# Performance work log

Hardware: AMD Instinct MI355X
Metric: run time of the kernel (lower is better)

Reference implementation:

```python
import jax, jax.numpy as jnp
import numpy as np

V, B, T, D, H, C = 50000, 64, 256, 256, 256, 32  # H = hidden_dim//2 per direction


def setup_inputs() -> dict:
    key = jax.random.key(0)
    ks = jax.random.split(key, 16)
    u = lambda k, s, a=0.1: jax.random.uniform(k, s, jnp.float32, -a, a)
    sc = 1.0 / float(np.sqrt(H))             # pytorch LSTM init range
    xav = float(np.sqrt(6.0 / (2 * H + C)))  # xavier_uniform for hidden2tag
    inp = {}
    inp['sentences'] = jax.random.randint(ks[0], (B, T), 1, V).astype(jnp.int32)
    inp['lengths'] = jax.random.randint(ks[1], (B,), 1, T + 1).astype(jnp.int32)
    inp['emb'] = u(ks[2], (V, D))
    inp['w_ih_f'] = u(ks[3], (4 * H, D), sc)
    inp['w_hh_f'] = u(ks[4], (4 * H, H), sc)
    inp['b_ih_f'] = u(ks[5], (4 * H,), sc)
    inp['b_hh_f'] = u(ks[6], (4 * H,), sc)
    inp['w_ih_b'] = u(ks[7], (4 * H, D), sc)
    inp['w_hh_b'] = u(ks[8], (4 * H, H), sc)
    inp['b_ih_b'] = u(ks[9], (4 * H,), sc)
    inp['b_hh_b'] = u(ks[10], (4 * H,), sc)
    inp['w_out'] = u(ks[11], (C, 2 * H), xav)
    inp['b_out'] = jnp.zeros((C,), jnp.float32)
    inp['start_trans'] = u(ks[12], (C,))
    inp['end_trans'] = u(ks[13], (C,))
    inp['trans'] = u(ks[14], (C, C))
    return inp


def _lstm(x, w_ih, w_hh, b_ih, b_hh):
    # x: [B,T,In] -> outputs [B,T,H]; PyTorch gate order i,f,g,o
    Bn, Hn = x.shape[0], w_hh.shape[1]

    def step(carry, x_t):
        h, c = carry
        g = x_t @ w_ih.T + h @ w_hh.T + (b_ih + b_hh)
        i, f, gg, o = jnp.split(g, 4, axis=-1)
        c = jax.nn.sigmoid(f) * c + jax.nn.sigmoid(i) * jnp.tanh(gg)
        h = jax.nn.sigmoid(o) * jnp.tanh(c)
        return (h, c), h

    init = (jnp.zeros((Bn, Hn), x.dtype), jnp.zeros((Bn, Hn), x.dtype))
    _, hs = jax.lax.scan(step, init, jnp.swapaxes(x, 0, 1))
    return jnp.swapaxes(hs, 0, 1)


def _emissions(sentences, lengths, emb, w_ih_f, w_hh_f, b_ih_f, b_hh_f,
               w_ih_b, w_hh_b, b_ih_b, b_hh_b, w_out, b_out):
    x = emb[sentences]                       # [B,T,D]
    Tn = x.shape[1]
    out_f = _lstm(x, w_ih_f, w_hh_f, b_ih_f, b_hh_f)
    # packed BiLSTM reverses each sequence within its own length
    t_idx = jnp.arange(Tn)
    rev = jnp.where(t_idx[None, :] < lengths[:, None],
                    lengths[:, None] - 1 - t_idx[None, :], t_idx[None, :])
    x_rev = jnp.take_along_axis(x, rev[:, :, None], axis=1)
    out_b = _lstm(x_rev, w_ih_b, w_hh_b, b_ih_b, b_hh_b)
    out_b = jnp.take_along_axis(out_b, rev[:, :, None], axis=1)  # rev is involution on valid region
    h = jnp.concatenate([out_f, out_b], axis=-1)  # [B,T,2H]
    return h @ w_out.T + b_out                    # [B,T,C]


def _viterbi(emissions, mask, lengths, start_trans, end_trans, trans):
    Bn, Tn, Cn = emissions.shape
    em = jnp.swapaxes(emissions, 0, 1)  # [T,B,C]
    mk = jnp.swapaxes(mask, 0, 1)       # [T,B]
    score0 = start_trans + em[0]

    def step(score, xs):
        emit_t, m_t = xs
        cand = score[:, :, None] + trans            # [B,C_prev,C_cur]
        best_prev = jnp.argmax(cand, axis=1)        # [B,C]
        new = jnp.where(m_t[:, None], jnp.max(cand, axis=1) + emit_t, score)
        return new, best_prev

    final, hist = jax.lax.scan(step, score0, (em[1:], mk[1:]))
    final = final + end_trans
    best_last = jnp.argmax(final, axis=1)           # [B]
    best_score = jnp.max(final, axis=1)             # [B]
    bidx = jnp.arange(Bn)

    def back(tag, xs):
        h_t, t = xs
        new = jnp.where(t < lengths - 1, h_t[bidx, tag], tag)
        return new, new

    _, tags = jax.lax.scan(back, best_last, (hist, jnp.arange(Tn - 1)), reverse=True)
    paths = jnp.concatenate([tags, best_last[None]], axis=0).T  # [B,T]; entries past length hold best_last
    return paths, best_score


def reference(sentences, lengths, emb, w_ih_f, w_hh_f, b_ih_f, b_hh_f,
              w_ih_b, w_hh_b, b_ih_b, b_hh_b, w_out, b_out,
              start_trans, end_trans, trans):
    mask = jnp.arange(sentences.shape[1])[None, :] < lengths[:, None]
    emissions = _emissions(sentences, lengths, emb, w_ih_f, w_hh_f, b_ih_f, b_hh_f,
                           w_ih_b, w_hh_b, b_ih_b, b_hh_b, w_out, b_out)
    return _viterbi(emissions, mask, lengths, start_trans, end_trans, trans)
```

## Files before the change

kernel.cpp:

```cpp
#include <hip/hip_runtime.h>
#include <math.h>


typedef unsigned long long ull;

__device__ __forceinline__ void bar_lds()
{
    asm volatile("s_waitcnt lgkmcnt(0)\n\ts_barrier" ::: "memory");
}

__global__ __launch_bounds__(256) void k1_xgemm(
    const int* __restrict__ sent, const int* __restrict__ lens,
    const float* __restrict__ emb,
    const float* __restrict__ wih_f, const float* __restrict__ wih_b,
    const float* __restrict__ bih_f, const float* __restrict__ bhh_f,
    const float* __restrict__ bih_b, const float* __restrict__ bhh_b,
    float* __restrict__ xg)
{
    const int bid = blockIdx.x;
    const int dir = bid >> 10;
    const int rem = bid & 1023;
    const int mt = rem >> 3, nt = rem & 7;
    const int r0 = mt * 128, j0 = nt * 128;
    const int b = r0 >> 8, t0 = r0 & 255;
    const float* __restrict__ wih = dir ? wih_b : wih_f;
    const float* __restrict__ bih = dir ? bih_b : bih_f;
    const float* __restrict__ bhh = dir ? bhh_b : bhh_f;

    __shared__ __align__(16) float At[32][132];
    __shared__ __align__(16) float Bt[32][132];
    __shared__ int tok_s[128];

    const int tid = threadIdx.x;
    if (tid < 128) {
        int t = t0 + tid;
        int tt = t;
        if (dir) { int L = lens[b]; if (t < L) tt = L - 1 - t; }
        tok_s[tid] = sent[b * 256 + tt];
    }
    __syncthreads();

    float acc[8][8];
    #pragma unroll
    for (int i = 0; i < 8; ++i)
        #pragma unroll
        for (int j = 0; j < 8; ++j) acc[i][j] = 0.f;

    const int lrow = tid >> 3;
    const int l8 = tid & 7;
    const int tx = tid & 15, ty = tid >> 4;

    for (int kc = 0; kc < 256; kc += 32) {
        #pragma unroll
        for (int it = 0; it < 4; ++it) {
            int row = lrow + it * 32;
            float4 va = *(const float4*)(emb + (size_t)tok_s[row] * 256 + kc + l8 * 4);
            At[l8*4+0][row] = va.x; At[l8*4+1][row] = va.y;
            At[l8*4+2][row] = va.z; At[l8*4+3][row] = va.w;
            float4 vb = *(const float4*)(wih + (size_t)(j0 + row) * 256 + kc + l8 * 4);
            Bt[l8*4+0][row] = vb.x; Bt[l8*4+1][row] = vb.y;
            Bt[l8*4+2][row] = vb.z; Bt[l8*4+3][row] = vb.w;
        }
        __syncthreads();
        #pragma unroll
        for (int k = 0; k < 32; ++k) {
            float4 a0 = *(const float4*)&At[k][ty*8];
            float4 a1 = *(const float4*)&At[k][ty*8+4];
            float4 b0 = *(const float4*)&Bt[k][tx*8];
            float4 b1 = *(const float4*)&Bt[k][tx*8+4];
            float av[8] = {a0.x,a0.y,a0.z,a0.w,a1.x,a1.y,a1.z,a1.w};
            float bv[8] = {b0.x,b0.y,b0.z,b0.w,b1.x,b1.y,b1.z,b1.w};
            #pragma unroll
            for (int i = 0; i < 8; ++i)
                #pragma unroll
                for (int j = 0; j < 8; ++j)
                    acc[i][j] += av[i] * bv[j];
        }
        __syncthreads();
    }

    float bias[8];
    {
        float4 p0 = *(const float4*)(bih + j0 + tx*8);
        float4 p1 = *(const float4*)(bih + j0 + tx*8 + 4);
        float4 q0 = *(const float4*)(bhh + j0 + tx*8);
        float4 q1 = *(const float4*)(bhh + j0 + tx*8 + 4);
        bias[0]=p0.x+q0.x; bias[1]=p0.y+q0.y; bias[2]=p0.z+q0.z; bias[3]=p0.w+q0.w;
        bias[4]=p1.x+q1.x; bias[5]=p1.y+q1.y; bias[6]=p1.z+q1.z; bias[7]=p1.w+q1.w;
    }
    #pragma unroll
    for (int i = 0; i < 8; ++i) {
        int r = r0 + ty*8 + i;
        int t = r & 255;
        float* orow = xg + ((size_t)(dir*64 + b) * 256 + t) * 1024 + j0 + tx*8;
        float4 o0, o1;
        o0.x = acc[i][0]+bias[0]; o0.y = acc[i][1]+bias[1];
        o0.z = acc[i][2]+bias[2]; o0.w = acc[i][3]+bias[3];
        o1.x = acc[i][4]+bias[4]; o1.y = acc[i][5]+bias[5];
        o1.z = acc[i][6]+bias[6]; o1.w = acc[i][7]+bias[7];
        *(float4*)orow = o0;
        *(float4*)(orow + 4) = o1;
    }
}

__global__ __launch_bounds__(512)
__attribute__((amdgpu_waves_per_eu(2, 2)))
void k2_lstm(
    const float* __restrict__ whh_f, const float* __restrict__ whh_b,
    const float* __restrict__ xg, float* __restrict__ hcat,
    ull* __restrict__ hx)
{
    const int m = blockIdx.x >> 6;
    const int g = blockIdx.x & 63;
    const int dir = g >> 5;
    const int b0 = (g & 31) * 2;
    const float* __restrict__ w = dir ? whh_b : whh_f;

    const int tid = threadIdx.x;
    const int kg = tid >> 6;
    const int q  = tid & 63;
    const int gate = q >> 4;
    const int u0 = (q & 15) * 4;
    const int kbase = kg * 32;
    const int j0 = gate * 256 + m * 64 + u0;

    float4 wv[4][8];
    #pragma unroll
    for (int j = 0; j < 4; ++j) {
        const float* wp = w + (size_t)(j0 + j) * 256 + kbase;
        #pragma unroll
        for (int i = 0; i < 8; ++i)
            wv[j][i] = *(const float4*)(wp + i * 4);
    }
    #pragma unroll
    for (int j = 0; j < 4; ++j)
        #pragma unroll
        for (int i = 0; i < 8; ++i)
            asm volatile("" : "+v"(wv[j][i].x), "+v"(wv[j][i].y),
                              "+v"(wv[j][i].z), "+v"(wv[j][i].w));

    __shared__ __align__(16) float hs[2][256];
    __shared__ __align__(16) float red[8][2][256];

    const int s_c = tid >> 6, ul = tid & 63;
    const float* xgp = xg + (size_t)(dir * 64 + b0 + s_c) * 262144 + m * 64 + ul;
    ull* hx_w = hx + ((size_t)g * 2 + s_c) * 256 + m * 64 + ul;
    float* hc_w = hcat + (size_t)(b0 + s_c) * 131072 + dir * 256 + m * 64 + ul;

    const int tid2 = tid - 256;
    const int s_r = tid2 >> 7, pr = tid2 & 127;
    const ull* hx_r = hx + ((size_t)g * 2 + s_r) * 256 + 2 * pr;

    ((float*)hs)[tid & 511] = 0.f;
    float c_reg = 0.f;
    bar_lds();

    for (int t = 0; t < 256; ++t) {
        const int par = t & 1;

        float xp0 = 0.f, xp1 = 0.f, xp2 = 0.f, xp3 = 0.f;
        if (tid < 128) {
            const float* xq = xgp + (size_t)t * 1024;
            xp0 = xq[0]; xp1 = xq[256]; xp2 = xq[512]; xp3 = xq[768];
        }

        float a0s0 = 0.f, a1s0 = 0.f, a2s0 = 0.f, a3s0 = 0.f;
        float a0s1 = 0.f, a1s1 = 0.f, a2s1 = 0.f, a3s1 = 0.f;
        #pragma unroll
        for (int i = 0; i < 8; ++i) {
            float4 ha = *(const float4*)&hs[0][kbase + i * 4];
            float4 hb = *(const float4*)&hs[1][kbase + i * 4];
            float4 w0 = wv[0][i], w1 = wv[1][i], w2 = wv[2][i], w3 = wv[3][i];
            a0s0 += w0.x*ha.x + w0.y*ha.y + w0.z*ha.z + w0.w*ha.w;
            a1s0 += w1.x*ha.x + w1.y*ha.y + w1.z*ha.z + w1.w*ha.w;
            a2s0 += w2.x*ha.x + w2.y*ha.y + w2.z*ha.z + w2.w*ha.w;
            a3s0 += w3.x*ha.x + w3.y*ha.y + w3.z*ha.z + w3.w*ha.w;
            a0s1 += w0.x*hb.x + w0.y*hb.y + w0.z*hb.z + w0.w*hb.w;
            a1s1 += w1.x*hb.x + w1.y*hb.y + w1.z*hb.z + w1.w*hb.w;
            a2s1 += w2.x*hb.x + w2.y*hb.y + w2.z*hb.z + w2.w*hb.w;
            a3s1 += w3.x*hb.x + w3.y*hb.y + w3.z*hb.z + w3.w*hb.w;
        }
        float4 r0v; r0v.x = a0s0; r0v.y = a1s0; r0v.z = a2s0; r0v.w = a3s0;
        float4 r1v; r1v.x = a0s1; r1v.y = a1s1; r1v.z = a2s1; r1v.w = a3s1;
        *(float4*)&red[kg][0][q * 4] = r0v;
        *(float4*)&red[kg][1][q * 4] = r1v;
        bar_lds();

        if (tid < 128) {
            float gi = xp0, gf = xp1, gg = xp2, go = xp3;
            #pragma unroll
            for (int kk = 0; kk < 8; ++kk) {
                gi += red[kk][s_c][ul];
                gf += red[kk][s_c][64 + ul];
                gg += red[kk][s_c][128 + ul];
                go += red[kk][s_c][192 + ul];
            }
            float si = 1.f / (1.f + expf(-gi));
            float sf = 1.f / (1.f + expf(-gf));
            float so = 1.f / (1.f + expf(-go));
            c_reg = sf * c_reg + si * tanhf(gg);
            float hn = so * tanhf(c_reg);
            ull pk = ((ull)(unsigned)(t + 1) << 32) | (ull)__float_as_uint(hn);
            __hip_atomic_store(hx_w + (size_t)par * 32768, pk,
                               __ATOMIC_RELAXED, __HIP_MEMORY_SCOPE_AGENT);
            hc_w[(size_t)t * 512] = hn;
        } else if (tid >= 256) {
            const unsigned tg = (unsigned)(t + 1);
            const ull* p = hx_r + (size_t)par * 32768;
            ull v0, v1;
            do {
                v0 = __hip_atomic_load(p,     __ATOMIC_RELAXED, __HIP_MEMORY_SCOPE_AGENT);
                v1 = __hip_atomic_load(p + 1, __ATOMIC_RELAXED, __HIP_MEMORY_SCOPE_AGENT);
            } while ((unsigned)(v0 >> 32) != tg || (unsigned)(v1 >> 32) != tg);
            hs[s_r][2 * pr]     = __uint_as_float((unsigned)v0);
            hs[s_r][2 * pr + 1] = __uint_as_float((unsigned)v1);
        }
        bar_lds();
    }
}

__global__ __launch_bounds__(256) void k3_emis(
    const float* __restrict__ hcat, const float* __restrict__ wout,
    const float* __restrict__ bout, const int* __restrict__ lens,
    float* __restrict__ em)
{
    const int b = blockIdx.x >> 3;
    const int tt0 = (blockIdx.x & 7) * 32;
    __shared__ float wsw[512 * 32];
    const int tid = threadIdx.x;
    for (int i = tid; i < 16384; i += 256) {
        int c_ = i >> 9, k_ = i & 511;
        wsw[k_ * 32 + ((k_ + c_) & 31)] = wout[i];
    }
    __syncthreads();
    const int c = tid & 31, tq = tid >> 5;
    const int L = lens[b];
    float acc[4];
    const float* hfp[4];
    const float* hbp[4];
    int tv[4];
    #pragma unroll
    for (int i = 0; i < 4; ++i) {
        int t = tt0 + i * 8 + tq;
        tv[i] = t;
        int tr = (t < L) ? (L - 1 - t) : t;
        hfp[i] = hcat + ((size_t)b * 256 + t) * 512;
        hbp[i] = hcat + ((size_t)b * 256 + tr) * 512 + 256;
        acc[i] = bout[c];
    }
    for (int k = 0; k < 256; k += 4) {
        float w0 = wsw[(k+0)*32 + ((k+0+c)&31)];
        float w1 = wsw[(k+1)*32 + ((k+1+c)&31)];
        float w2_ = wsw[(k+2)*32 + ((k+2+c)&31)];
        float w3 = wsw[(k+3)*32 + ((k+3+c)&31)];
        #pragma unroll
        for (int i = 0; i < 4; ++i) {
            float4 h = *(const float4*)(hfp[i] + k);
            acc[i] += h.x*w0 + h.y*w1 + h.z*w2_ + h.w*w3;
        }
        float v0 = wsw[(256+k+0)*32 + ((256+k+0+c)&31)];
        float v1 = wsw[(256+k+1)*32 + ((256+k+1+c)&31)];
        float v2 = wsw[(256+k+2)*32 + ((256+k+2+c)&31)];
        float v3 = wsw[(256+k+3)*32 + ((256+k+3+c)&31)];
        #pragma unroll
        for (int i = 0; i < 4; ++i) {
            float4 h = *(const float4*)(hbp[i] + k);
            acc[i] += h.x*v0 + h.y*v1 + h.z*v2 + h.w*v3;
        }
    }
    #pragma unroll
    for (int i = 0; i < 4; ++i)
        em[((size_t)b * 256 + tv[i]) * 32 + c] = acc[i];
}

__global__ __launch_bounds__(256) void k4_viterbi(
    const float* __restrict__ em, const int* __restrict__ lens,
    const float* __restrict__ strans, const float* __restrict__ etrans,
    const float* __restrict__ trans, float* __restrict__ out)
{
    const int b = blockIdx.x;
    __shared__ float em_s[8192];
    __shared__ float trans_t[32 * 33];
    __shared__ float score_s[32];
    __shared__ float fin[32];
    __shared__ unsigned char hist[256][32];
    __shared__ unsigned char path[256];
    __shared__ float bs_s;
    const int tid = threadIdx.x;
    for (int i = tid; i < 8192; i += 256) em_s[i] = em[(size_t)b * 8192 + i];
    for (int i = tid; i < 1024; i += 256) {
        int p = i >> 5, cc = i & 31;
        trans_t[cc * 33 + p] = trans[i];
    }
    __syncthreads();
    if (tid < 32) score_s[tid] = strans[tid] + em_s[tid];
    __syncthreads();
    const int c = tid >> 3, pg = tid & 7;
    const int L = lens[b];
    for (int t = 1; t < 256; ++t) {
        float v = -1e30f; int bi = 0;
        #pragma unroll
        for (int i = 0; i < 4; ++i) {
            int p = pg * 4 + i;
            float cand = score_s[p] + trans_t[c * 33 + p];
            if (cand > v) { v = cand; bi = p; }
        }
        #pragma unroll
        for (int off = 4; off >= 1; off >>= 1) {
            float ov = __shfl_down(v, off);
            int oi = __shfl_down(bi, off);
            if (ov > v) { v = ov; bi = oi; }
        }
        float ns = 0.f;
        if (pg == 0) {
            hist[t][c] = (unsigned char)bi;
            ns = (t < L) ? (v + em_s[t * 32 + c]) : score_s[c];
        }
        __syncthreads();
        if (pg == 0) score_s[c] = ns;
        __syncthreads();
    }
    if (tid < 32) fin[tid] = score_s[tid] + etrans[tid];
    __syncthreads();
    if (tid == 0) {
        float bv = -1e30f; int bl = 0;
        for (int cc = 0; cc < 32; ++cc)
            if (fin[cc] > bv) { bv = fin[cc]; bl = cc; }
        bs_s = bv;
        int tag = bl;
        path[255] = (unsigned char)tag;
        for (int t = 254; t >= 0; --t) {
            if (t < L - 1) tag = hist[t + 1][tag];
            path[t] = (unsigned char)tag;
        }
    }
    __syncthreads();
    out[(size_t)b * 256 + tid] = (float)path[tid];
    if (tid == 0) out[16384 + b] = bs_s;
}

extern "C" void kernel_launch(void* const* d_in, const int* in_sizes, int n_in,
                              void* d_out, int out_size, void* d_ws, size_t ws_size,
                              hipStream_t stream)
{
    const int*   sent   = (const int*)  d_in[0];
    const int*   lens   = (const int*)  d_in[1];
    const float* emb    = (const float*)d_in[2];
    const float* wih_f  = (const float*)d_in[3];
    const float* whh_f  = (const float*)d_in[4];
    const float* bih_f  = (const float*)d_in[5];
    const float* bhh_f  = (const float*)d_in[6];
    const float* wih_b  = (const float*)d_in[7];
    const float* whh_b  = (const float*)d_in[8];
    const float* bih_b  = (const float*)d_in[9];
    const float* bhh_b  = (const float*)d_in[10];
    const float* wout   = (const float*)d_in[11];
    const float* bout   = (const float*)d_in[12];
    const float* strans = (const float*)d_in[13];
    const float* etrans = (const float*)d_in[14];
    const float* trans  = (const float*)d_in[15];
    float* out = (float*)d_out;

    float* ws   = (float*)d_ws;
    float* xg   = ws;
    float* hcat = xg + 33554432;
    float* em   = hcat + 8388608;
    ull*   hx   = (ull*)(em + 524288);

    hipLaunchKernelGGL(k1_xgemm, dim3(2048), dim3(256), 0, stream,
                       sent, lens, emb, wih_f, wih_b, bih_f, bhh_f, bih_b, bhh_b, xg);
    hipLaunchKernelGGL(k2_lstm, dim3(256), dim3(512), 0, stream,
                       whh_f, whh_b, xg, hcat, hx);
    hipLaunchKernelGGL(k3_emis, dim3(512), dim3(256), 0, stream,
                       hcat, wout, bout, lens, em);
    hipLaunchKernelGGL(k4_viterbi, dim3(64), dim3(256), 0, stream,
                       em, lens, strans, etrans, trans, out);
}
```

Baseline: 1.017 ms.

## Process four sequences per LSTM block and halve the recurrent grid

The persistent recurrent LSTM kernel now handles four batch rows per block instead of two. Each block reuses its register-resident W_hh slice across twice as many sequences, and the grid shrinks from 256 to 128 blocks, which reduces the number of blocks spinning on the cross-block hidden-state exchange. Sigmoid and tanh are rewritten as explicit exp-based formulas to make the gate math cheaper. In exchange, each block does double the per-step work on its critical path and uses more LDS. The exp-based tanh may also lose some accuracy.

```diff
diff --git a/kernel.cpp b/kernel.cpp
--- a/kernel.cpp
+++ b/kernel.cpp
@@ -8,6 +8,9 @@
 {
     asm volatile("s_waitcnt lgkmcnt(0)\n\ts_barrier" ::: "memory");
 }
+
+__device__ __forceinline__ float sigm(float x) { return 1.f / (1.f + expf(-x)); }
+__device__ __forceinline__ float tanh_f(float x) { return 1.f - 2.f / (expf(2.f * x) + 1.f); }
 
 __global__ __launch_bounds__(256) void k1_xgemm(
     const int* __restrict__ sent, const int* __restrict__ lens,
@@ -110,10 +113,10 @@
     const float* __restrict__ xg, float* __restrict__ hcat,
     ull* __restrict__ hx)
 {
-    const int m = blockIdx.x >> 6;
-    const int g = blockIdx.x & 63;
-    const int dir = g >> 5;
-    const int b0 = (g & 31) * 2;
+    const int m = blockIdx.x >> 5;
+    const int g = blockIdx.x & 31;
+    const int dir = g >> 4;
+    const int b0 = (g & 15) * 4;
     const float* __restrict__ w = dir ? whh_b : whh_f;
 
     const int tid = threadIdx.x;
@@ -139,19 +142,20 @@
             asm volatile("" : "+v"(wv[j][i].x), "+v"(wv[j][i].y),
                               "+v"(wv[j][i].z), "+v"(wv[j][i].w));
 
-    __shared__ __align__(16) float hs[2][256];
-    __shared__ __align__(16) float red[8][2][256];
+    __shared__ __align__(16) float hs[4][256];
+    __shared__ __align__(16) float red[8][4][256];
 
     const int s_c = tid >> 6, ul = tid & 63;
     const float* xgp = xg + (size_t)(dir * 64 + b0 + s_c) * 262144 + m * 64 + ul;
-    ull* hx_w = hx + ((size_t)g * 2 + s_c) * 256 + m * 64 + ul;
+    ull* hx_w = hx + ((size_t)g * 4 + s_c) * 256 + m * 64 + ul;
     float* hc_w = hcat + (size_t)(b0 + s_c) * 131072 + dir * 256 + m * 64 + ul;
 
     const int tid2 = tid - 256;
-    const int s_r = tid2 >> 7, pr = tid2 & 127;
-    const ull* hx_r = hx + ((size_t)g * 2 + s_r) * 256 + 2 * pr;
+    const int s_r = tid2 >> 6, pr = tid2 & 63;
+    const ull* hx_r = hx + ((size_t)g * 4 + s_r) * 256 + 4 * pr;
 
     ((float*)hs)[tid & 511] = 0.f;
+    ((float*)hs)[512 + (tid & 511)] = 0.f;
     float c_reg = 0.f;
     bar_lds();
 
@@ -159,34 +163,39 @@
         const int par = t & 1;
 
         float xp0 = 0.f, xp1 = 0.f, xp2 = 0.f, xp3 = 0.f;
-        if (tid < 128) {
+        if (tid < 256) {
             const float* xq = xgp + (size_t)t * 1024;
             xp0 = xq[0]; xp1 = xq[256]; xp2 = xq[512]; xp3 = xq[768];
         }
 
-        float a0s0 = 0.f, a1s0 = 0.f, a2s0 = 0.f, a3s0 = 0.f;
-        float a0s1 = 0.f, a1s1 = 0.f, a2s1 = 0.f, a3s1 = 0.f;
+        float a[4][4];
+        #pragma unroll
+        for (int r = 0; r < 4; ++r)
+            #pragma unroll
+            for (int s = 0; s < 4; ++s) a[r][s] = 0.f;
         #pragma unroll
         for (int i = 0; i < 8; ++i) {
-            float4 ha = *(const float4*)&hs[0][kbase + i * 4];
-            float4 hb = *(const float4*)&hs[1][kbase + i * 4];
-            float4 w0 = wv[0][i], w1 = wv[1][i], w2 = wv[2][i], w3 = wv[3][i];
-            a0s0 += w0.x*ha.x + w0.y*ha.y + w0.z*ha.z + w0.w*ha.w;
-            a1s0 += w1.x*ha.x + w1.y*ha.y + w1.z*ha.z + w1.w*ha.w;
-            a2s0 += w2.x*ha.x + w2.y*ha.y + w2.z*ha.z + w2.w*ha.w;
-            a3s0 += w3.x*ha.x + w3.y*ha.y + w3.z*ha.z + w3.w*ha.w;
-            a0s1 += w0.x*hb.x + w0.y*hb.y + w0.z*hb.z + w0.w*hb.w;
-            a1s1 += w1.x*hb.x + w1.y*hb.y + w1.z*hb.z + w1.w*hb.w;
-            a2s1 += w2.x*hb.x + w2.y*hb.y + w2.z*hb.z + w2.w*hb.w;
-            a3s1 += w3.x*hb.x + w3.y*hb.y + w3.z*hb.z + w3.w*hb.w;
-        }
-        float4 r0v; r0v.x = a0s0; r0v.y = a1s0; r0v.z = a2s0; r0v.w = a3s0;
-        float4 r1v; r1v.x = a0s1; r1v.y = a1s1; r1v.z = a2s1; r1v.w = a3s1;
-        *(float4*)&red[kg][0][q * 4] = r0v;
-        *(float4*)&red[kg][1][q * 4] = r1v;
+            float4 h0 = *(const float4*)&hs[0][kbase + i * 4];
+            float4 h1 = *(const float4*)&hs[1][kbase + i * 4];
+            float4 h2 = *(const float4*)&hs[2][kbase + i * 4];
+            float4 h3 = *(const float4*)&hs[3][kbase + i * 4];
+            #pragma unroll
+            for (int r = 0; r < 4; ++r) {
+                float4 wr = wv[r][i];
+                a[r][0] += wr.x*h0.x + wr.y*h0.y + wr.z*h0.z + wr.w*h0.w;
+                a[r][1] += wr.x*h1.x + wr.y*h1.y + wr.z*h1.z + wr.w*h1.w;
+                a[r][2] += wr.x*h2.x + wr.y*h2.y + wr.z*h2.z + wr.w*h2.w;
+                a[r][3] += wr.x*h3.x + wr.y*h3.y + wr.z*h3.z + wr.w*h3.w;
+            }
+        }
+        #pragma unroll
+        for (int s = 0; s < 4; ++s) {
+            float4 rv; rv.x = a[0][s]; rv.y = a[1][s]; rv.z = a[2][s]; rv.w = a[3][s];
+            *(float4*)&red[kg][s][q * 4] = rv;
+        }
         bar_lds();
 
-        if (tid < 128) {
+        if (tid < 256) {
             float gi = xp0, gf = xp1, gg = xp2, go = xp3;
             #pragma unroll
             for (int kk = 0; kk < 8; ++kk) {
@@ -195,25 +204,30 @@
                 gg += red[kk][s_c][128 + ul];
                 go += red[kk][s_c][192 + ul];
             }
-            float si = 1.f / (1.f + expf(-gi));
-            float sf = 1.f / (1.f + expf(-gf));
-            float so = 1.f / (1.f + expf(-go));
-            c_reg = sf * c_reg + si * tanhf(gg);
-            float hn = so * tanhf(c_reg);
+            float si = sigm(gi);
+            float sf = sigm(gf);
+            float so = sigm(go);
+            c_reg = sf * c_reg + si * tanh_f(gg);
+            float hn = so * tanh_f(c_reg);
             ull pk = ((ull)(unsigned)(t + 1) << 32) | (ull)__float_as_uint(hn);
             __hip_atomic_store(hx_w + (size_t)par * 32768, pk,
                                __ATOMIC_RELAXED, __HIP_MEMORY_SCOPE_AGENT);
             hc_w[(size_t)t * 512] = hn;
-        } else if (tid >= 256) {
+        } else {
             const unsigned tg = (unsigned)(t + 1);
             const ull* p = hx_r + (size_t)par * 32768;
-            ull v0, v1;
+            ull v0, v1, v2, v3;
             do {
                 v0 = __hip_atomic_load(p,     __ATOMIC_RELAXED, __HIP_MEMORY_SCOPE_AGENT);
                 v1 = __hip_atomic_load(p + 1, __ATOMIC_RELAXED, __HIP_MEMORY_SCOPE_AGENT);
-            } while ((unsigned)(v0 >> 32) != tg || (unsigned)(v1 >> 32) != tg);
-            hs[s_r][2 * pr]     = __uint_as_float((unsigned)v0);
-            hs[s_r][2 * pr + 1] = __uint_as_float((unsigned)v1);
+                v2 = __hip_atomic_load(p + 2, __ATOMIC_RELAXED, __HIP_MEMORY_SCOPE_AGENT);
+                v3 = __hip_atomic_load(p + 3, __ATOMIC_RELAXED, __HIP_MEMORY_SCOPE_AGENT);
+            } while ((unsigned)(v0 >> 32) != tg || (unsigned)(v1 >> 32) != tg ||
+                     (unsigned)(v2 >> 32) != tg || (unsigned)(v3 >> 32) != tg);
+            hs[s_r][4 * pr]     = __uint_as_float((unsigned)v0);
+            hs[s_r][4 * pr + 1] = __uint_as_float((unsigned)v1);
+            hs[s_r][4 * pr + 2] = __uint_as_float((unsigned)v2);
+            hs[s_r][4 * pr + 3] = __uint_as_float((unsigned)v3);
         }
         bar_lds();
     }
@@ -369,7 +383,7 @@
 
     hipLaunchKernelGGL(k1_xgemm, dim3(2048), dim3(256), 0, stream,
                        sent, lens, emb, wih_f, wih_b, bih_f, bhh_f, bih_b, bhh_b, xg);
-    hipLaunchKernelGGL(k2_lstm, dim3(256), dim3(512), 0, stream,
+    hipLaunchKernelGGL(k2_lstm, dim3(128), dim3(512), 0, stream,
                        whh_f, whh_b, xg, hcat, hx);
     hipLaunchKernelGGL(k3_emis, dim3(512), dim3(256), 0, stream,
                        hcat, wout, bout, lens, em);
```

Result: slower. 1.282 ms (+26.1%).
